# Kernel optimization log

Measured on AMD Instinct MI355X. Metric: run time of the kernel, lower is better.

## Reference

```python
import jax, jax.numpy as jnp
import numpy as np

N_NODES = 100000
N_EDGES = 1600000
IN_FEATS = 128
N_HIDDEN = 128
N_CLASSES = 64


def _degree_norms(src, dst, n_nodes):
    ones = jnp.ones(src.shape[0], dtype=jnp.float32)
    deg_out = jax.ops.segment_sum(ones, src, num_segments=n_nodes)  # out-degree of src nodes
    deg_in = jax.ops.segment_sum(ones, dst, num_segments=n_nodes)   # in-degree of dst nodes
    norm_src = jax.lax.rsqrt(jnp.clip(deg_out, 1.0))  # D_src^{-1/2}, clamp like DGL
    norm_dst = jax.lax.rsqrt(jnp.clip(deg_in, 1.0))   # D_dst^{-1/2}
    return norm_src, norm_dst


def _graph_conv(x, src, dst, norm_src, norm_dst, W, b, relu):
    # DGL GraphConv, norm='both': D_dst^{-1/2} A D_src^{-1/2} X W + b
    h = x * norm_src[:, None]
    agg = jax.ops.segment_sum(h[src], dst, num_segments=x.shape[0])  # [N, d]
    h = agg * norm_dst[:, None]
    h = h @ W + b
    return jax.nn.relu(h) if relu else h


def setup_inputs() -> dict:
    key = jax.random.key(0)
    ks = jax.random.split(key, 10)
    features = jax.random.normal(ks[0], (N_NODES, IN_FEATS), dtype=jnp.float32)
    src = jax.random.randint(ks[1], (N_EDGES,), 0, N_NODES, dtype=jnp.int64 if jax.config.read('jax_enable_x64') else jnp.int32)
    dst = jax.random.randint(ks[2], (N_EDGES,), 0, N_NODES, dtype=src.dtype)
    s = 1.0 / np.sqrt(IN_FEATS)
    W0 = jax.random.uniform(ks[3], (IN_FEATS, N_HIDDEN), jnp.float32, -s, s)
    b0 = jnp.zeros((N_HIDDEN,), jnp.float32)
    sh = 1.0 / np.sqrt(N_HIDDEN)
    W1 = jax.random.uniform(ks[4], (N_HIDDEN, N_HIDDEN), jnp.float32, -sh, sh)
    b1 = jnp.zeros((N_HIDDEN,), jnp.float32)
    W2 = jax.random.uniform(ks[5], (N_HIDDEN, N_CLASSES), jnp.float32, -sh, sh)
    b2 = jnp.zeros((N_CLASSES,), jnp.float32)
    return {"features": features, "src": src, "dst": dst,
            "W0": W0, "b0": b0, "W1": W1, "b1": b1, "W2": W2, "b2": b2}


def reference(features, src, dst, W0, b0, W1, b1, W2, b2):
    norm_src, norm_dst = _degree_norms(src, dst, features.shape[0])
    # dropout is identity in eval mode
    h = _graph_conv(features, src, dst, norm_src, norm_dst, W0, b0, relu=True)
    h = _graph_conv(h, src, dst, norm_src, norm_dst, W1, b1, relu=True)
    h = _graph_conv(h, src, dst, norm_src, norm_dst, W2, b2, relu=False)
    return h
```

## Files before the change

### kernel.cpp

```cpp
#include <hip/hip_runtime.h>
#include <hip/hip_fp16.h>

#define K_FEATS 128
#define RBSHIFT 9
#define RB 512

typedef short bf16x8 __attribute__((ext_vector_type(8)));
typedef float f32x4 __attribute__((ext_vector_type(4)));

__device__ __forceinline__ unsigned short bf16_rne(float x) {
    unsigned u = __float_as_uint(x);
    unsigned r = (u + 0x7FFFu + ((u >> 16) & 1u)) >> 16;
    return (unsigned short)r;
}
__device__ __forceinline__ float bf16_f(unsigned short h) {
    return __uint_as_float(((unsigned)h) << 16);
}

__global__ __launch_bounds__(256) void split_feat(
    const float* __restrict__ X, unsigned short* __restrict__ Xh,
    unsigned short* __restrict__ Xl, int n, int n_pad)
{
    size_t idx = ((size_t)blockIdx.x * 256 + threadIdx.x) * 4;
    if (idx >= (size_t)n_pad * K_FEATS) return;
    int row = (int)(idx >> 7);
    float4 v = make_float4(0.f, 0.f, 0.f, 0.f);
    if (row < n) v = *(const float4*)(X + idx);
    float f[4] = {v.x, v.y, v.z, v.w};
    union { ushort4 q; unsigned short u[4]; } H, L;
#pragma unroll
    for (int j = 0; j < 4; j++) {
        H.u[j] = bf16_rne(f[j]);
        L.u[j] = bf16_rne(f[j] - bf16_f(H.u[j]));
    }
    *(ushort4*)(Xh + idx) = H.q;
    *(ushort4*)(Xl + idx) = L.q;
}

__global__ __launch_bounds__(256) void split_w3(
    const float* __restrict__ W0, const float* __restrict__ W1,
    const float* __restrict__ W2,
    unsigned short* __restrict__ W0th, unsigned short* __restrict__ W0tl,
    unsigned short* __restrict__ W1th, unsigned short* __restrict__ W1tl,
    unsigned short* __restrict__ W2th, unsigned short* __restrict__ W2tl)
{
    int e = blockIdx.x * 256 + threadIdx.x;
    const float* W;
    unsigned short *Wh, *Wl;
    int NC, idx;
    if (e < 16384)      { W = W0; Wh = W0th; Wl = W0tl; NC = 128; idx = e; }
    else if (e < 32768) { W = W1; Wh = W1th; Wl = W1tl; NC = 128; idx = e - 16384; }
    else if (e < 40960) { W = W2; Wh = W2th; Wl = W2tl; NC = 64;  idx = e - 32768; }
    else return;
    int c = idx >> 7, k = idx & 127;
    float w = W[k * NC + c];
    unsigned short h = bf16_rne(w);
    Wh[idx] = h;
    Wl[idx] = bf16_rne(w - bf16_f(h));
}

__global__ __launch_bounds__(256) void bucket_count(
    const int* __restrict__ src, const int* __restrict__ dst,
    int* __restrict__ partialS, int* __restrict__ partialD,
    int ne, int chunkA, int C, int NB)
{
    __shared__ int h[256];
    int c = blockIdx.x, t = threadIdx.x;
    const int* key = blockIdx.y ? dst : src;
    int* part = blockIdx.y ? partialD : partialS;
    if (t < NB) h[t] = 0;
    __syncthreads();
    int e0 = c * chunkA, e1 = min(ne, e0 + chunkA);
    for (int e = e0 + t; e < e1; e += 256)
        atomicAdd(&h[key[e] >> RBSHIFT], 1);
    __syncthreads();
    for (int i = t; i < NB; i += 256) part[i * C + c] = h[i];
}

__global__ __launch_bounds__(256) void bucket_prefix(
    int* __restrict__ partialS, int* __restrict__ partialD,
    int* __restrict__ totS, int* __restrict__ totD, int C, int NB)
{
    __shared__ int sh[256];
    int b = blockIdx.x, t = threadIdx.x;
    int* part = blockIdx.y ? partialD : partialS;
    int* tot = blockIdx.y ? totD : totS;
    int v = (t < C) ? part[b * C + t] : 0;
    sh[t] = v;
    __syncthreads();
    for (int off = 1; off < 256; off <<= 1) {
        int x = (t >= off) ? sh[t - off] : 0;
        __syncthreads();
        sh[t] += x;
        __syncthreads();
    }
    if (t < C) part[b * C + t] = sh[t] - v;
    if (t == 255) tot[b] = sh[255];
}

__global__ __launch_bounds__(256) void bucket_off_kernel(
    const int* __restrict__ totS, const int* __restrict__ totD,
    int* __restrict__ offS, int* __restrict__ offD,
    int* __restrict__ row_off, int NB, int n, int ne)
{
    __shared__ int sh[256];
    int t = threadIdx.x;
    if (t == 0) row_off[n] = ne;
    for (int a = 0; a < 2; a++) {
        const int* tot = a ? totD : totS;
        int* boff = a ? offD : offS;
        int v = (t < NB) ? tot[t] : 0;
        sh[t] = v;
        __syncthreads();
        for (int off = 1; off < 256; off <<= 1) {
            int x = (t >= off) ? sh[t - off] : 0;
            __syncthreads();
            sh[t] += x;
            __syncthreads();
        }
        if (t < NB) boff[t] = sh[t] - v;
        if (t == NB - 1) boff[NB] = sh[t];
        __syncthreads();
    }
}

__global__ __launch_bounds__(256) void bucket_scatter(
    const int* __restrict__ src, const int* __restrict__ dst,
    const int* __restrict__ partialS, const int* __restrict__ partialD,
    const int* __restrict__ offS, const int* __restrict__ offD,
    unsigned short* __restrict__ src_bkt, int* __restrict__ edge_bkt,
    int ne, int chunkA, int C, int NB)
{
    __shared__ int curS[256];
    __shared__ int curD[256];
    int c = blockIdx.x, t = threadIdx.x;
    if (t < NB) {
        curS[t] = offS[t] + partialS[t * C + c];
        curD[t] = offD[t] + partialD[t * C + c];
    }
    __syncthreads();
    int e0 = c * chunkA, e1 = min(ne, e0 + chunkA);
    for (int e = e0 + t; e < e1; e += 256) {
        int s = src[e];
        int d = dst[e];
        int posD = atomicAdd(&curD[d >> RBSHIFT], 1);
        edge_bkt[posD] = ((d & (RB - 1)) << 17) | s;
        int posS = atomicAdd(&curS[s >> RBSHIFT], 1);
        src_bkt[posS] = (unsigned short)(s & (RB - 1));
    }
}

__global__ __launch_bounds__(256) void fine_all(
    const int* __restrict__ edge_bkt, const unsigned short* __restrict__ src_bkt,
    const int* __restrict__ offD, const int* __restrict__ offS,
    int* __restrict__ row_off, float* __restrict__ norm_dst,
    float* __restrict__ norm_src, int* __restrict__ csr, int n)
{
    __shared__ int h[RB];
    __shared__ int ps[256];
    int b = blockIdx.x, t = threadIdx.x;
    int lo = b << RBSHIFT;
    for (int i = t; i < RB; i += 256) h[i] = 0;
    __syncthreads();
    if (blockIdx.y == 1) {
        int e1 = offS[b + 1];
        for (int e = offS[b] + t; e < e1; e += 256)
            atomicAdd(&h[src_bkt[e]], 1);
        __syncthreads();
        for (int i = t; i < RB; i += 256) {
            int g = lo + i;
            if (g < n) norm_src[g] = rsqrtf((float)max(h[i], 1));
        }
        return;
    }
    int ebase = offD[b];
    int e1 = offD[b + 1];
    for (int e = ebase + t; e < e1; e += 256)
        atomicAdd(&h[(unsigned)edge_bkt[e] >> 17], 1);
    __syncthreads();
    int v0 = h[2 * t], v1 = h[2 * t + 1];
    ps[t] = v0 + v1;
    __syncthreads();
    for (int off = 1; off < 256; off <<= 1) {
        int x = (t >= off) ? ps[t - off] : 0;
        __syncthreads();
        ps[t] += x;
        __syncthreads();
    }
    int excl = ps[t] - (v0 + v1) + ebase;
    int g0 = lo + 2 * t, g1 = g0 + 1;
    if (g0 < n) { row_off[g0] = excl;      norm_dst[g0] = rsqrtf((float)max(v0, 1)); }
    if (g1 < n) { row_off[g1] = excl + v0; norm_dst[g1] = rsqrtf((float)max(v1, 1)); }
    h[2 * t] = excl;
    h[2 * t + 1] = excl + v0;
    __syncthreads();
    for (int e = ebase + t; e < e1; e += 256) {
        int p = edge_bkt[e];
        int pos = atomicAdd(&h[(unsigned)p >> 17], 1);
        csr[pos] = p & 0x1FFFF;
    }
}

template <int NCOL, bool HALF_OUT>
__global__ __launch_bounds__(256) void gemm_mfma(
    const unsigned short* __restrict__ Xh, const unsigned short* __restrict__ Xl,
    const unsigned short* __restrict__ Wth, const unsigned short* __restrict__ Wtl,
    const float* __restrict__ scale, void* __restrict__ outv, int n)
{
    constexpr int CT = NCOL / 16;
    constexpr int CHUNKS = NCOL * 16;
    __shared__ unsigned short Ws[16 * NCOL * 8];

    int t = threadIdx.x;
    int w = t >> 6, lane = t & 63, m = lane & 15, q = lane >> 4;
    int r0 = blockIdx.x * 128 + w * 32;

    f32x4 acc[2][CT];
#pragma unroll
    for (int i = 0; i < 2; i++)
#pragma unroll
        for (int j = 0; j < CT; j++) acc[i][j] = (f32x4){0.f, 0.f, 0.f, 0.f};

    size_t aoff0 = (size_t)(r0 + m) * K_FEATS + q * 8;
    size_t aoff1 = aoff0 + (size_t)16 * K_FEATS;

    bf16x8 ah[2][4], al[2][4];
#pragma unroll
    for (int k = 0; k < 4; k++) {
        ah[0][k] = *(const bf16x8*)(Xh + aoff0 + k * 32);
        ah[1][k] = *(const bf16x8*)(Xh + aoff1 + k * 32);
        al[0][k] = *(const bf16x8*)(Xl + aoff0 + k * 32);
        al[1][k] = *(const bf16x8*)(Xl + aoff1 + k * 32);
    }

#pragma unroll
    for (int i = 0; i < CHUNKS / 256; i++) {
        int g = t + i * 256;
        int col = g >> 4, sec = g & 15;
        *(bf16x8*)(Ws + sec * NCOL * 8 + ((col ^ (sec & 7)) * 8)) =
            *(const bf16x8*)(Wth + g * 8);
    }
    __syncthreads();
#pragma unroll
    for (int k = 0; k < 4; k++) {
        int sec = k * 4 + q;
#pragma unroll
        for (int ct = 0; ct < CT; ct++) {
            bf16x8 bh = *(const bf16x8*)(Ws + sec * NCOL * 8 +
                                         (((ct * 16 + m) ^ (sec & 7)) * 8));
            acc[0][ct] = __builtin_amdgcn_mfma_f32_16x16x32_bf16(ah[0][k], bh, acc[0][ct], 0, 0, 0);
            acc[0][ct] = __builtin_amdgcn_mfma_f32_16x16x32_bf16(al[0][k], bh, acc[0][ct], 0, 0, 0);
            acc[1][ct] = __builtin_amdgcn_mfma_f32_16x16x32_bf16(ah[1][k], bh, acc[1][ct], 0, 0, 0);
            acc[1][ct] = __builtin_amdgcn_mfma_f32_16x16x32_bf16(al[1][k], bh, acc[1][ct], 0, 0, 0);
        }
    }
    __syncthreads();
#pragma unroll
    for (int i = 0; i < CHUNKS / 256; i++) {
        int g = t + i * 256;
        int col = g >> 4, sec = g & 15;
        *(bf16x8*)(Ws + sec * NCOL * 8 + ((col ^ (sec & 7)) * 8)) =
            *(const bf16x8*)(Wtl + g * 8);
    }
    __syncthreads();
#pragma unroll
    for (int k = 0; k < 4; k++) {
        int sec = k * 4 + q;
#pragma unroll
        for (int ct = 0; ct < CT; ct++) {
            bf16x8 bl = *(const bf16x8*)(Ws + sec * NCOL * 8 +
                                         (((ct * 16 + m) ^ (sec & 7)) * 8));
            acc[0][ct] = __builtin_amdgcn_mfma_f32_16x16x32_bf16(ah[0][k], bl, acc[0][ct], 0, 0, 0);
            acc[1][ct] = __builtin_amdgcn_mfma_f32_16x16x32_bf16(ah[1][k], bl, acc[1][ct], 0, 0, 0);
        }
    }

#pragma unroll
    for (int rt = 0; rt < 2; rt++) {
        int rb = r0 + rt * 16 + q * 4;
#pragma unroll
        for (int reg = 0; reg < 4; reg++) {
            int row = rb + reg;
            if (row < n) {
                float s = scale[row];
#pragma unroll
                for (int ct = 0; ct < CT; ct++) {
                    float v = acc[rt][ct][reg] * s;
                    size_t o = (size_t)row * NCOL + ct * 16 + m;
                    if (HALF_OUT) ((__half*)outv)[o] = __float2half(v);
                    else ((float*)outv)[o] = v;
                }
            }
        }
    }
}

template <bool RELU>
__global__ __launch_bounds__(256) void aggregate4h(
    const __half* __restrict__ Tm, const int* __restrict__ row_off,
    const int* __restrict__ csr, const float* __restrict__ ndst,
    const float* __restrict__ bias, unsigned short* __restrict__ Oh,
    unsigned short* __restrict__ Ol, int n)
{
    int lane = threadIdx.x & 15;
    int team = threadIdx.x >> 4;
    int fb = lane * 8;
    float b[8];
    *(float4*)&b[0] = *(const float4*)(bias + fb);
    *(float4*)&b[4] = *(const float4*)(bias + fb + 4);
    int stride = gridDim.x * 16;
    for (int v = blockIdx.x * 16 + team; v < n; v += stride) {
        int s = row_off[v], e = row_off[v + 1];
        float nd = ndst[v];
        float a[8] = {};
        int i = s;
        for (; i + 4 <= e; i += 4) {
            int u0 = csr[i], u1 = csr[i + 1], u2 = csr[i + 2], u3 = csr[i + 3];
            union { uint4 q; __half h[8]; } U0, U1, U2, U3;
            U0.q = *(const uint4*)(Tm + (size_t)u0 * 128 + fb);
            U1.q = *(const uint4*)(Tm + (size_t)u1 * 128 + fb);
            U2.q = *(const uint4*)(Tm + (size_t)u2 * 128 + fb);
            U3.q = *(const uint4*)(Tm + (size_t)u3 * 128 + fb);
#pragma unroll
            for (int j = 0; j < 8; j++)
                a[j] += (__half2float(U0.h[j]) + __half2float(U1.h[j])) +
                        (__half2float(U2.h[j]) + __half2float(U3.h[j]));
        }
        for (; i < e; i++) {
            int u = csr[i];
            union { uint4 q; __half h[8]; } U;
            U.q = *(const uint4*)(Tm + (size_t)u * 128 + fb);
#pragma unroll
            for (int j = 0; j < 8; j++) a[j] += __half2float(U.h[j]);
        }
        union { uint4 q; unsigned short u[8]; } H, L;
#pragma unroll
        for (int j = 0; j < 8; j++) {
            float o = nd * a[j] + b[j];
            if (RELU) o = fmaxf(o, 0.f);
            H.u[j] = bf16_rne(o);
            L.u[j] = bf16_rne(o - bf16_f(H.u[j]));
        }
        *(uint4*)(Oh + (size_t)v * 128 + fb) = H.q;
        *(uint4*)(Ol + (size_t)v * 128 + fb) = L.q;
    }
}

template <bool RELU>
__global__ __launch_bounds__(256) void aggregate2(
    const float* __restrict__ Tm, const int* __restrict__ row_off,
    const int* __restrict__ csr, const float* __restrict__ ndst,
    const float* __restrict__ bias, float* __restrict__ out, int n)
{
    int lane = threadIdx.x & 15;
    int team = threadIdx.x >> 4;
    int fb = lane * 4;
    float4 b = *(const float4*)(bias + fb);
    int stride = gridDim.x * 16;
    for (int v = blockIdx.x * 16 + team; v < n; v += stride) {
        int s = row_off[v], e = row_off[v + 1];
        float nd = ndst[v];
        float ax = 0.f, ay = 0.f, az = 0.f, aw = 0.f;
        int i = s;
        for (; i + 4 <= e; i += 4) {
            int u0 = csr[i], u1 = csr[i + 1], u2 = csr[i + 2], u3 = csr[i + 3];
            float4 t0 = *(const float4*)(Tm + (size_t)u0 * 64 + fb);
            float4 t1 = *(const float4*)(Tm + (size_t)u1 * 64 + fb);
            float4 t2 = *(const float4*)(Tm + (size_t)u2 * 64 + fb);
            float4 t3 = *(const float4*)(Tm + (size_t)u3 * 64 + fb);
            ax += (t0.x + t1.x) + (t2.x + t3.x);
            ay += (t0.y + t1.y) + (t2.y + t3.y);
            az += (t0.z + t1.z) + (t2.z + t3.z);
            aw += (t0.w + t1.w) + (t2.w + t3.w);
        }
        for (; i < e; i++) {
            int u = csr[i];
            float4 t0 = *(const float4*)(Tm + (size_t)u * 64 + fb);
            ax += t0.x; ay += t0.y; az += t0.z; aw += t0.w;
        }
        float4 o;
        o.x = nd * ax + b.x;
        o.y = nd * ay + b.y;
        o.z = nd * az + b.z;
        o.w = nd * aw + b.w;
        if (RELU) {
            o.x = fmaxf(o.x, 0.f); o.y = fmaxf(o.y, 0.f);
            o.z = fmaxf(o.z, 0.f); o.w = fmaxf(o.w, 0.f);
        }
        *(float4*)(out + (size_t)v * 64 + fb) = o;
    }
}

extern "C" void kernel_launch(void* const* d_in, const int* in_sizes, int n_in,
                              void* d_out, int out_size, void* d_ws, size_t ws_size,
                              hipStream_t stream)
{
    const float* features = (const float*)d_in[0];
    const int* src = (const int*)d_in[1];
    const int* dst = (const int*)d_in[2];
    const float* W0 = (const float*)d_in[3];
    const float* b0 = (const float*)d_in[4];
    const float* W1 = (const float*)d_in[5];
    const float* b1 = (const float*)d_in[6];
    const float* W2 = (const float*)d_in[7];
    const float* b2 = (const float*)d_in[8];

    int n = in_sizes[0] / K_FEATS;
    int ne = in_sizes[1];
    int n_pad = (n + 127) & ~127;

    char* ws = (char*)d_ws;
    size_t off = 0;
    auto take = [&](size_t bytes) -> char* {
        char* p = ws + off;
        off = (off + bytes + 255) & ~(size_t)255;
        return p;
    };
    unsigned short* XBh = (unsigned short*)take((size_t)n_pad * 128 * 2);
    unsigned short* XBl = (unsigned short*)take((size_t)n_pad * 128 * 2);
    char* Tbuf = take((size_t)n_pad * 128 * 2);
    int* csr = (int*)take((size_t)ne * 4);
    int* edge_bkt = (int*)take((size_t)ne * 4);
    unsigned short* src_bkt = (unsigned short*)take((size_t)ne * 2);
    int* row_off = (int*)take((size_t)(n + 1) * 4);
    float* norm_src = (float*)take((size_t)n * 4);
    float* norm_dst = (float*)take((size_t)n * 4);
    unsigned short* W0th = (unsigned short*)take(128 * 128 * 2);
    unsigned short* W0tl = (unsigned short*)take(128 * 128 * 2);
    unsigned short* W1th = (unsigned short*)take(128 * 128 * 2);
    unsigned short* W1tl = (unsigned short*)take(128 * 128 * 2);
    unsigned short* W2th = (unsigned short*)take(64 * 128 * 2);
    unsigned short* W2tl = (unsigned short*)take(64 * 128 * 2);

    int NB = (n + RB - 1) >> RBSHIFT;
    int chunkA = 8192;
    int C = (ne + chunkA - 1) / chunkA;
    if (C > 256) { chunkA = (ne + 255) / 256; C = (ne + chunkA - 1) / chunkA; }

    int* partialS = (int*)take((size_t)NB * C * 4);
    int* partialD = (int*)take((size_t)NB * C * 4);
    int* totS = (int*)take((size_t)NB * 4);
    int* totD = (int*)take((size_t)NB * 4);
    int* offS = (int*)take((size_t)(NB + 1) * 4);
    int* offD = (int*)take((size_t)(NB + 1) * 4);

    int fblocks = (int)(((size_t)n_pad * 128 / 4 + 255) / 256);
    split_feat<<<fblocks, 256, 0, stream>>>(features, XBh, XBl, n, n_pad);
    split_w3<<<160, 256, 0, stream>>>(W0, W1, W2, W0th, W0tl, W1th, W1tl, W2th, W2tl);

    bucket_count<<<dim3(C, 2), 256, 0, stream>>>(src, dst, partialS, partialD,
                                                 ne, chunkA, C, NB);
    bucket_prefix<<<dim3(NB, 2), 256, 0, stream>>>(partialS, partialD, totS, totD, C, NB);
    bucket_off_kernel<<<1, 256, 0, stream>>>(totS, totD, offS, offD, row_off, NB, n, ne);
    bucket_scatter<<<C, 256, 0, stream>>>(src, dst, partialS, partialD,
                                          offS, offD, src_bkt, edge_bkt,
                                          ne, chunkA, C, NB);
    fine_all<<<dim3(NB, 2), 256, 0, stream>>>(edge_bkt, src_bkt, offD, offS,
                                              row_off, norm_dst, norm_src, csr, n);

    int gblocks = n_pad / 128;
    int ablocks = (n + 15) / 16;
    __half* Th = (__half*)Tbuf;
    float* T64 = (float*)Tbuf;

    gemm_mfma<128, true><<<gblocks, 256, 0, stream>>>(XBh, XBl, W0th, W0tl,
                                                      norm_src, Th, n);
    aggregate4h<true><<<ablocks, 256, 0, stream>>>(Th, row_off, csr, norm_dst, b0,
                                                   XBh, XBl, n);
    gemm_mfma<128, true><<<gblocks, 256, 0, stream>>>(XBh, XBl, W1th, W1tl,
                                                      norm_src, Th, n);
    aggregate4h<true><<<ablocks, 256, 0, stream>>>(Th, row_off, csr, norm_dst, b1,
                                                   XBh, XBl, n);
    gemm_mfma<64, false><<<gblocks, 256, 0, stream>>>(XBh, XBl, W2th, W2tl,
                                                      norm_src, T64, n);
    aggregate2<false><<<ablocks, 256, 0, stream>>>(T64, row_off, csr, norm_dst, b2,
                                                   (float*)d_out, n);
}
```

Measured before the change: 427.2 us.

## Fuse feature split into first GEMM and slice aggregation by feature columns

```diff
diff --git a/kernel.cpp b/kernel.cpp
--- a/kernel.cpp
+++ b/kernel.cpp
@@ -15,26 +15,6 @@
 }
 __device__ __forceinline__ float bf16_f(unsigned short h) {
     return __uint_as_float(((unsigned)h) << 16);
-}
-
-__global__ __launch_bounds__(256) void split_feat(
-    const float* __restrict__ X, unsigned short* __restrict__ Xh,
-    unsigned short* __restrict__ Xl, int n, int n_pad)
-{
-    size_t idx = ((size_t)blockIdx.x * 256 + threadIdx.x) * 4;
-    if (idx >= (size_t)n_pad * K_FEATS) return;
-    int row = (int)(idx >> 7);
-    float4 v = make_float4(0.f, 0.f, 0.f, 0.f);
-    if (row < n) v = *(const float4*)(X + idx);
-    float f[4] = {v.x, v.y, v.z, v.w};
-    union { ushort4 q; unsigned short u[4]; } H, L;
-#pragma unroll
-    for (int j = 0; j < 4; j++) {
-        H.u[j] = bf16_rne(f[j]);
-        L.u[j] = bf16_rne(f[j] - bf16_f(H.u[j]));
-    }
-    *(ushort4*)(Xh + idx) = H.q;
-    *(ushort4*)(Xl + idx) = L.q;
 }
 
 __global__ __launch_bounds__(256) void split_w3(
@@ -201,9 +181,10 @@
     }
 }
 
-template <int NCOL, bool HALF_OUT>
+template <int NCOL, bool HALF_OUT, bool F32IN>
 __global__ __launch_bounds__(256) void gemm_mfma(
     const unsigned short* __restrict__ Xh, const unsigned short* __restrict__ Xl,
+    const float* __restrict__ Xf,
     const unsigned short* __restrict__ Wth, const unsigned short* __restrict__ Wtl,
     const float* __restrict__ scale, void* __restrict__ outv, int n)
 {
@@ -221,16 +202,43 @@
 #pragma unroll
         for (int j = 0; j < CT; j++) acc[i][j] = (f32x4){0.f, 0.f, 0.f, 0.f};
 
-    size_t aoff0 = (size_t)(r0 + m) * K_FEATS + q * 8;
-    size_t aoff1 = aoff0 + (size_t)16 * K_FEATS;
-
     bf16x8 ah[2][4], al[2][4];
-#pragma unroll
-    for (int k = 0; k < 4; k++) {
-        ah[0][k] = *(const bf16x8*)(Xh + aoff0 + k * 32);
-        ah[1][k] = *(const bf16x8*)(Xh + aoff1 + k * 32);
-        al[0][k] = *(const bf16x8*)(Xl + aoff0 + k * 32);
-        al[1][k] = *(const bf16x8*)(Xl + aoff1 + k * 32);
+    if (F32IN) {
+#pragma unroll
+        for (int rt = 0; rt < 2; rt++) {
+            int row = r0 + rt * 16 + m;
+            bool ok = row < n;
+            size_t base = (size_t)row * K_FEATS + q * 8;
+#pragma unroll
+            for (int k = 0; k < 4; k++) {
+                float f[8];
+                if (ok) {
+                    *(float4*)&f[0] = *(const float4*)(Xf + base + k * 32);
+                    *(float4*)&f[4] = *(const float4*)(Xf + base + k * 32 + 4);
+                } else {
+#pragma unroll
+                    for (int j = 0; j < 8; j++) f[j] = 0.f;
+                }
+                union { bf16x8 v; unsigned short u[8]; } H, L;
+#pragma unroll
+                for (int j = 0; j < 8; j++) {
+                    H.u[j] = bf16_rne(f[j]);
+                    L.u[j] = bf16_rne(f[j] - bf16_f(H.u[j]));
+                }
+                ah[rt][k] = H.v;
+                al[rt][k] = L.v;
+            }
+        }
+    } else {
+        size_t aoff0 = (size_t)(r0 + m) * K_FEATS + q * 8;
+        size_t aoff1 = aoff0 + (size_t)16 * K_FEATS;
+#pragma unroll
+        for (int k = 0; k < 4; k++) {
+            ah[0][k] = *(const bf16x8*)(Xh + aoff0 + k * 32);
+            ah[1][k] = *(const bf16x8*)(Xh + aoff1 + k * 32);
+            al[0][k] = *(const bf16x8*)(Xl + aoff0 + k * 32);
+            al[1][k] = *(const bf16x8*)(Xl + aoff1 + k * 32);
+        }
     }
 
 #pragma unroll
@@ -295,99 +303,69 @@
     }
 }
 
-template <bool RELU>
-__global__ __launch_bounds__(256) void aggregate4h(
+template <int NCOL, int SLICES, bool RELU, bool BF16_OUT>
+__global__ __launch_bounds__(256) void aggregate_sliced(
     const __half* __restrict__ Tm, const int* __restrict__ row_off,
     const int* __restrict__ csr, const float* __restrict__ ndst,
-    const float* __restrict__ bias, unsigned short* __restrict__ Oh,
-    unsigned short* __restrict__ Ol, int n)
-{
-    int lane = threadIdx.x & 15;
-    int team = threadIdx.x >> 4;
-    int fb = lane * 8;
-    float b[8];
-    *(float4*)&b[0] = *(const float4*)(bias + fb);
-    *(float4*)&b[4] = *(const float4*)(bias + fb + 4);
-    int stride = gridDim.x * 16;
-    for (int v = blockIdx.x * 16 + team; v < n; v += stride) {
-        int s = row_off[v], e = row_off[v + 1];
-        float nd = ndst[v];
-        float a[8] = {};
-        int i = s;
-        for (; i + 4 <= e; i += 4) {
-            int u0 = csr[i], u1 = csr[i + 1], u2 = csr[i + 2], u3 = csr[i + 3];
-            union { uint4 q; __half h[8]; } U0, U1, U2, U3;
-            U0.q = *(const uint4*)(Tm + (size_t)u0 * 128 + fb);
-            U1.q = *(const uint4*)(Tm + (size_t)u1 * 128 + fb);
-            U2.q = *(const uint4*)(Tm + (size_t)u2 * 128 + fb);
-            U3.q = *(const uint4*)(Tm + (size_t)u3 * 128 + fb);
-#pragma unroll
-            for (int j = 0; j < 8; j++)
-                a[j] += (__half2float(U0.h[j]) + __half2float(U1.h[j])) +
-                        (__half2float(U2.h[j]) + __half2float(U3.h[j]));
-        }
-        for (; i < e; i++) {
-            int u = csr[i];
-            union { uint4 q; __half h[8]; } U;
-            U.q = *(const uint4*)(Tm + (size_t)u * 128 + fb);
-#pragma unroll
-            for (int j = 0; j < 8; j++) a[j] += __half2float(U.h[j]);
-        }
-        union { uint4 q; unsigned short u[8]; } H, L;
-#pragma unroll
-        for (int j = 0; j < 8; j++) {
-            float o = nd * a[j] + b[j];
-            if (RELU) o = fmaxf(o, 0.f);
-            H.u[j] = bf16_rne(o);
-            L.u[j] = bf16_rne(o - bf16_f(H.u[j]));
-        }
-        *(uint4*)(Oh + (size_t)v * 128 + fb) = H.q;
-        *(uint4*)(Ol + (size_t)v * 128 + fb) = L.q;
-    }
-}
-
-template <bool RELU>
-__global__ __launch_bounds__(256) void aggregate2(
-    const float* __restrict__ Tm, const int* __restrict__ row_off,
-    const int* __restrict__ csr, const float* __restrict__ ndst,
-    const float* __restrict__ bias, float* __restrict__ out, int n)
-{
-    int lane = threadIdx.x & 15;
-    int team = threadIdx.x >> 4;
-    int fb = lane * 4;
-    float4 b = *(const float4*)(bias + fb);
-    int stride = gridDim.x * 16;
-    for (int v = blockIdx.x * 16 + team; v < n; v += stride) {
-        int s = row_off[v], e = row_off[v + 1];
-        float nd = ndst[v];
-        float ax = 0.f, ay = 0.f, az = 0.f, aw = 0.f;
-        int i = s;
-        for (; i + 4 <= e; i += 4) {
-            int u0 = csr[i], u1 = csr[i + 1], u2 = csr[i + 2], u3 = csr[i + 3];
-            float4 t0 = *(const float4*)(Tm + (size_t)u0 * 64 + fb);
-            float4 t1 = *(const float4*)(Tm + (size_t)u1 * 64 + fb);
-            float4 t2 = *(const float4*)(Tm + (size_t)u2 * 64 + fb);
-            float4 t3 = *(const float4*)(Tm + (size_t)u3 * 64 + fb);
-            ax += (t0.x + t1.x) + (t2.x + t3.x);
-            ay += (t0.y + t1.y) + (t2.y + t3.y);
-            az += (t0.z + t1.z) + (t2.z + t3.z);
-            aw += (t0.w + t1.w) + (t2.w + t3.w);
-        }
-        for (; i < e; i++) {
-            int u = csr[i];
-            float4 t0 = *(const float4*)(Tm + (size_t)u * 64 + fb);
-            ax += t0.x; ay += t0.y; az += t0.z; aw += t0.w;
-        }
-        float4 o;
-        o.x = nd * ax + b.x;
-        o.y = nd * ay + b.y;
-        o.z = nd * az + b.z;
-        o.w = nd * aw + b.w;
-        if (RELU) {
-            o.x = fmaxf(o.x, 0.f); o.y = fmaxf(o.y, 0.f);
-            o.z = fmaxf(o.z, 0.f); o.w = fmaxf(o.w, 0.f);
-        }
-        *(float4*)(out + (size_t)v * 64 + fb) = o;
+    const float* __restrict__ bias, void* __restrict__ outA,
+    unsigned short* __restrict__ outB, int n)
+{
+    constexpr int SH = (SLICES == 8) ? 3 : 2;
+    int slice = blockIdx.x & (SLICES - 1);
+    int g = blockIdx.x >> SH;
+    int team = threadIdx.x >> 2;
+    int li = threadIdx.x & 3;
+    int fb = slice * 16 + li * 4;
+    int v = g * 64 + team;
+    if (v >= n) return;
+    float4 bb = *(const float4*)(bias + fb);
+    int s = row_off[v], e = row_off[v + 1];
+    float nd = ndst[v];
+    float a0 = 0.f, a1 = 0.f, a2 = 0.f, a3 = 0.f;
+    int i = s;
+    for (; i + 4 <= e; i += 4) {
+        int u0 = csr[i], u1 = csr[i + 1], u2 = csr[i + 2], u3 = csr[i + 3];
+        union { uint2 q; __half h[4]; } U0, U1, U2, U3;
+        U0.q = *(const uint2*)(Tm + (size_t)u0 * NCOL + fb);
+        U1.q = *(const uint2*)(Tm + (size_t)u1 * NCOL + fb);
+        U2.q = *(const uint2*)(Tm + (size_t)u2 * NCOL + fb);
+        U3.q = *(const uint2*)(Tm + (size_t)u3 * NCOL + fb);
+        a0 += (__half2float(U0.h[0]) + __half2float(U1.h[0])) +
+              (__half2float(U2.h[0]) + __half2float(U3.h[0]));
+        a1 += (__half2float(U0.h[1]) + __half2float(U1.h[1])) +
+              (__half2float(U2.h[1]) + __half2float(U3.h[1]));
+        a2 += (__half2float(U0.h[2]) + __half2float(U1.h[2])) +
+              (__half2float(U2.h[2]) + __half2float(U3.h[2]));
+        a3 += (__half2float(U0.h[3]) + __half2float(U1.h[3])) +
+              (__half2float(U2.h[3]) + __half2float(U3.h[3]));
+    }
+    for (; i < e; i++) {
+        int u = csr[i];
+        union { uint2 q; __half h[4]; } U;
+        U.q = *(const uint2*)(Tm + (size_t)u * NCOL + fb);
+        a0 += __half2float(U.h[0]);
+        a1 += __half2float(U.h[1]);
+        a2 += __half2float(U.h[2]);
+        a3 += __half2float(U.h[3]);
+    }
+    float o0 = nd * a0 + bb.x, o1 = nd * a1 + bb.y;
+    float o2 = nd * a2 + bb.z, o3 = nd * a3 + bb.w;
+    if (RELU) {
+        o0 = fmaxf(o0, 0.f); o1 = fmaxf(o1, 0.f);
+        o2 = fmaxf(o2, 0.f); o3 = fmaxf(o3, 0.f);
+    }
+    if (BF16_OUT) {
+        union { uint2 q; unsigned short u[4]; } H, L;
+        float o[4] = {o0, o1, o2, o3};
+#pragma unroll
+        for (int j = 0; j < 4; j++) {
+            H.u[j] = bf16_rne(o[j]);
+            L.u[j] = bf16_rne(o[j] - bf16_f(H.u[j]));
+        }
+        *(uint2*)((unsigned short*)outA + (size_t)v * NCOL + fb) = H.q;
+        *(uint2*)(outB + (size_t)v * NCOL + fb) = L.q;
+    } else {
+        *(float4*)((float*)outA + (size_t)v * NCOL + fb) = make_float4(o0, o1, o2, o3);
     }
 }
 
@@ -444,8 +422,6 @@
     int* offS = (int*)take((size_t)(NB + 1) * 4);
     int* offD = (int*)take((size_t)(NB + 1) * 4);
 
-    int fblocks = (int)(((size_t)n_pad * 128 / 4 + 255) / 256);
-    split_feat<<<fblocks, 256, 0, stream>>>(features, XBh, XBl, n, n_pad);
     split_w3<<<160, 256, 0, stream>>>(W0, W1, W2, W0th, W0tl, W1th, W1tl, W2th, W2tl);
 
     bucket_count<<<dim3(C, 2), 256, 0, stream>>>(src, dst, partialS, partialD,
@@ -459,20 +435,19 @@
                                               row_off, norm_dst, norm_src, csr, n);
 
     int gblocks = n_pad / 128;
-    int ablocks = (n + 15) / 16;
+    int ngroups = (n + 63) / 64;
     __half* Th = (__half*)Tbuf;
-    float* T64 = (float*)Tbuf;
-
-    gemm_mfma<128, true><<<gblocks, 256, 0, stream>>>(XBh, XBl, W0th, W0tl,
-                                                      norm_src, Th, n);
-    aggregate4h<true><<<ablocks, 256, 0, stream>>>(Th, row_off, csr, norm_dst, b0,
-                                                   XBh, XBl, n);
-    gemm_mfma<128, true><<<gblocks, 256, 0, stream>>>(XBh, XBl, W1th, W1tl,
-                                                      norm_src, Th, n);
-    aggregate4h<true><<<ablocks, 256, 0, stream>>>(Th, row_off, csr, norm_dst, b1,
-                                                   XBh, XBl, n);
-    gemm_mfma<64, false><<<gblocks, 256, 0, stream>>>(XBh, XBl, W2th, W2tl,
-                                                      norm_src, T64, n);
-    aggregate2<false><<<ablocks, 256, 0, stream>>>(T64, row_off, csr, norm_dst, b2,
-                                                   (float*)d_out, n);
-}
+
+    gemm_mfma<128, true, true><<<gblocks, 256, 0, stream>>>(
+        nullptr, nullptr, features, W0th, W0tl, norm_src, Th, n);
+    aggregate_sliced<128, 8, true, true><<<ngroups * 8, 256, 0, stream>>>(
+        Th, row_off, csr, norm_dst, b0, XBh, XBl, n);
+    gemm_mfma<128, true, false><<<gblocks, 256, 0, stream>>>(
+        XBh, XBl, nullptr, W1th, W1tl, norm_src, Th, n);
+    aggregate_sliced<128, 8, true, true><<<ngroups * 8, 256, 0, stream>>>(
+        Th, row_off, csr, norm_dst, b1, XBh, XBl, n);
+    gemm_mfma<64, true, false><<<gblocks, 256, 0, stream>>>(
+        XBh, XBl, nullptr, W2th, W2tl, norm_src, Th, n);
+    aggregate_sliced<64, 4, false, false><<<ngroups * 4, 256, 0, stream>>>(
+        Th, row_off, csr, norm_dst, b2, d_out, nullptr, n);
+}
```

After: 749.0 us. 75.3% more time.

## Fuse bf16 split into GEMM loads and store fp16 intermediates

Applied to the files above, without the earlier changes.

```diff
diff --git a/kernel.cpp b/kernel.cpp
--- a/kernel.cpp
+++ b/kernel.cpp
@@ -15,26 +15,6 @@
 }
 __device__ __forceinline__ float bf16_f(unsigned short h) {
     return __uint_as_float(((unsigned)h) << 16);
-}
-
-__global__ __launch_bounds__(256) void split_feat(
-    const float* __restrict__ X, unsigned short* __restrict__ Xh,
-    unsigned short* __restrict__ Xl, int n, int n_pad)
-{
-    size_t idx = ((size_t)blockIdx.x * 256 + threadIdx.x) * 4;
-    if (idx >= (size_t)n_pad * K_FEATS) return;
-    int row = (int)(idx >> 7);
-    float4 v = make_float4(0.f, 0.f, 0.f, 0.f);
-    if (row < n) v = *(const float4*)(X + idx);
-    float f[4] = {v.x, v.y, v.z, v.w};
-    union { ushort4 q; unsigned short u[4]; } H, L;
-#pragma unroll
-    for (int j = 0; j < 4; j++) {
-        H.u[j] = bf16_rne(f[j]);
-        L.u[j] = bf16_rne(f[j] - bf16_f(H.u[j]));
-    }
-    *(ushort4*)(Xh + idx) = H.q;
-    *(ushort4*)(Xl + idx) = L.q;
 }
 
 __global__ __launch_bounds__(256) void split_w3(
@@ -64,17 +44,21 @@
     int* __restrict__ partialS, int* __restrict__ partialD,
     int ne, int chunkA, int C, int NB)
 {
-    __shared__ int h[256];
+    __shared__ int hS[256];
+    __shared__ int hD[256];
     int c = blockIdx.x, t = threadIdx.x;
-    const int* key = blockIdx.y ? dst : src;
-    int* part = blockIdx.y ? partialD : partialS;
-    if (t < NB) h[t] = 0;
+    if (t < NB) { hS[t] = 0; hD[t] = 0; }
     __syncthreads();
     int e0 = c * chunkA, e1 = min(ne, e0 + chunkA);
-    for (int e = e0 + t; e < e1; e += 256)
-        atomicAdd(&h[key[e] >> RBSHIFT], 1);
-    __syncthreads();
-    for (int i = t; i < NB; i += 256) part[i * C + c] = h[i];
+    for (int e = e0 + t; e < e1; e += 256) {
+        atomicAdd(&hS[src[e] >> RBSHIFT], 1);
+        atomicAdd(&hD[dst[e] >> RBSHIFT], 1);
+    }
+    __syncthreads();
+    for (int i = t; i < NB; i += 256) {
+        partialS[i * C + c] = hS[i];
+        partialD[i * C + c] = hD[i];
+    }
 }
 
 __global__ __launch_bounds__(256) void bucket_prefix(
@@ -201,9 +185,9 @@
     }
 }
 
-template <int NCOL, bool HALF_OUT>
+template <int NCOL, bool HALF_OUT, int MODE>
 __global__ __launch_bounds__(256) void gemm_mfma(
-    const unsigned short* __restrict__ Xh, const unsigned short* __restrict__ Xl,
+    const __half* __restrict__ X16, const float* __restrict__ Xf,
     const unsigned short* __restrict__ Wth, const unsigned short* __restrict__ Wtl,
     const float* __restrict__ scale, void* __restrict__ outv, int n)
 {
@@ -221,16 +205,37 @@
 #pragma unroll
         for (int j = 0; j < CT; j++) acc[i][j] = (f32x4){0.f, 0.f, 0.f, 0.f};
 
-    size_t aoff0 = (size_t)(r0 + m) * K_FEATS + q * 8;
-    size_t aoff1 = aoff0 + (size_t)16 * K_FEATS;
-
     bf16x8 ah[2][4], al[2][4];
 #pragma unroll
-    for (int k = 0; k < 4; k++) {
-        ah[0][k] = *(const bf16x8*)(Xh + aoff0 + k * 32);
-        ah[1][k] = *(const bf16x8*)(Xh + aoff1 + k * 32);
-        al[0][k] = *(const bf16x8*)(Xl + aoff0 + k * 32);
-        al[1][k] = *(const bf16x8*)(Xl + aoff1 + k * 32);
+    for (int rt = 0; rt < 2; rt++) {
+        int row = r0 + rt * 16 + m;
+        size_t base = (size_t)row * K_FEATS + q * 8;
+#pragma unroll
+        for (int k = 0; k < 4; k++) {
+            float f[8];
+            if (MODE == 0) {
+                if (row < n) {
+                    *(float4*)&f[0] = *(const float4*)(Xf + base + k * 32);
+                    *(float4*)&f[4] = *(const float4*)(Xf + base + k * 32 + 4);
+                } else {
+#pragma unroll
+                    for (int j = 0; j < 8; j++) f[j] = 0.f;
+                }
+            } else {
+                union { uint4 q4; __half h[8]; } U;
+                U.q4 = *(const uint4*)(X16 + base + k * 32);
+#pragma unroll
+                for (int j = 0; j < 8; j++) f[j] = __half2float(U.h[j]);
+            }
+            union { bf16x8 v; unsigned short u[8]; } H, L;
+#pragma unroll
+            for (int j = 0; j < 8; j++) {
+                H.u[j] = bf16_rne(f[j]);
+                L.u[j] = bf16_rne(f[j] - bf16_f(H.u[j]));
+            }
+            ah[rt][k] = H.v;
+            al[rt][k] = L.v;
+        }
     }
 
 #pragma unroll
@@ -299,8 +304,7 @@
 __global__ __launch_bounds__(256) void aggregate4h(
     const __half* __restrict__ Tm, const int* __restrict__ row_off,
     const int* __restrict__ csr, const float* __restrict__ ndst,
-    const float* __restrict__ bias, unsigned short* __restrict__ Oh,
-    unsigned short* __restrict__ Ol, int n)
+    const float* __restrict__ bias, __half* __restrict__ Oh, int n)
 {
     int lane = threadIdx.x & 15;
     int team = threadIdx.x >> 4;
@@ -333,61 +337,58 @@
 #pragma unroll
             for (int j = 0; j < 8; j++) a[j] += __half2float(U.h[j]);
         }
-        union { uint4 q; unsigned short u[8]; } H, L;
+        union { uint4 q; __half h[8]; } O;
 #pragma unroll
         for (int j = 0; j < 8; j++) {
             float o = nd * a[j] + b[j];
             if (RELU) o = fmaxf(o, 0.f);
-            H.u[j] = bf16_rne(o);
-            L.u[j] = bf16_rne(o - bf16_f(H.u[j]));
-        }
-        *(uint4*)(Oh + (size_t)v * 128 + fb) = H.q;
-        *(uint4*)(Ol + (size_t)v * 128 + fb) = L.q;
-    }
-}
-
-template <bool RELU>
-__global__ __launch_bounds__(256) void aggregate2(
-    const float* __restrict__ Tm, const int* __restrict__ row_off,
+            O.h[j] = __float2half(o);
+        }
+        *(uint4*)(Oh + (size_t)v * 128 + fb) = O.q;
+    }
+}
+
+__global__ __launch_bounds__(256) void aggregate2h(
+    const __half* __restrict__ Tm, const int* __restrict__ row_off,
     const int* __restrict__ csr, const float* __restrict__ ndst,
     const float* __restrict__ bias, float* __restrict__ out, int n)
 {
-    int lane = threadIdx.x & 15;
-    int team = threadIdx.x >> 4;
-    int fb = lane * 4;
-    float4 b = *(const float4*)(bias + fb);
-    int stride = gridDim.x * 16;
-    for (int v = blockIdx.x * 16 + team; v < n; v += stride) {
+    int lane = threadIdx.x & 7;
+    int team = threadIdx.x >> 3;
+    int fb = lane * 8;
+    float b[8];
+    *(float4*)&b[0] = *(const float4*)(bias + fb);
+    *(float4*)&b[4] = *(const float4*)(bias + fb + 4);
+    int stride = gridDim.x * 32;
+    for (int v = blockIdx.x * 32 + team; v < n; v += stride) {
         int s = row_off[v], e = row_off[v + 1];
         float nd = ndst[v];
-        float ax = 0.f, ay = 0.f, az = 0.f, aw = 0.f;
+        float a[8] = {};
         int i = s;
         for (; i + 4 <= e; i += 4) {
             int u0 = csr[i], u1 = csr[i + 1], u2 = csr[i + 2], u3 = csr[i + 3];
-            float4 t0 = *(const float4*)(Tm + (size_t)u0 * 64 + fb);
-            float4 t1 = *(const float4*)(Tm + (size_t)u1 * 64 + fb);
-            float4 t2 = *(const float4*)(Tm + (size_t)u2 * 64 + fb);
-            float4 t3 = *(const float4*)(Tm + (size_t)u3 * 64 + fb);
-            ax += (t0.x + t1.x) + (t2.x + t3.x);
-            ay += (t0.y + t1.y) + (t2.y + t3.y);
-            az += (t0.z + t1.z) + (t2.z + t3.z);
-            aw += (t0.w + t1.w) + (t2.w + t3.w);
+            union { uint4 q; __half h[8]; } U0, U1, U2, U3;
+            U0.q = *(const uint4*)(Tm + (size_t)u0 * 64 + fb);
+            U1.q = *(const uint4*)(Tm + (size_t)u1 * 64 + fb);
+            U2.q = *(const uint4*)(Tm + (size_t)u2 * 64 + fb);
+            U3.q = *(const uint4*)(Tm + (size_t)u3 * 64 + fb);
+#pragma unroll
+            for (int j = 0; j < 8; j++)
+                a[j] += (__half2float(U0.h[j]) + __half2float(U1.h[j])) +
+                        (__half2float(U2.h[j]) + __half2float(U3.h[j]));
         }
         for (; i < e; i++) {
             int u = csr[i];
-            float4 t0 = *(const float4*)(Tm + (size_t)u * 64 + fb);
-            ax += t0.x; ay += t0.y; az += t0.z; aw += t0.w;
-        }
-        float4 o;
-        o.x = nd * ax + b.x;
-        o.y = nd * ay + b.y;
-        o.z = nd * az + b.z;
-        o.w = nd * aw + b.w;
-        if (RELU) {
-            o.x = fmaxf(o.x, 0.f); o.y = fmaxf(o.y, 0.f);
-            o.z = fmaxf(o.z, 0.f); o.w = fmaxf(o.w, 0.f);
-        }
-        *(float4*)(out + (size_t)v * 64 + fb) = o;
+            union { uint4 q; __half h[8]; } U;
+            U.q = *(const uint4*)(Tm + (size_t)u * 64 + fb);
+#pragma unroll
+            for (int j = 0; j < 8; j++) a[j] += __half2float(U.h[j]);
+        }
+        float o[8];
+#pragma unroll
+        for (int j = 0; j < 8; j++) o[j] = nd * a[j] + b[j];
+        *(float4*)(out + (size_t)v * 64 + fb) = *(float4*)&o[0];
+        *(float4*)(out + (size_t)v * 64 + fb + 4) = *(float4*)&o[4];
     }
 }
 
@@ -416,9 +417,8 @@
         off = (off + bytes + 255) & ~(size_t)255;
         return p;
     };
-    unsigned short* XBh = (unsigned short*)take((size_t)n_pad * 128 * 2);
-    unsigned short* XBl = (unsigned short*)take((size_t)n_pad * 128 * 2);
-    char* Tbuf = take((size_t)n_pad * 128 * 2);
+    __half* Xbuf = (__half*)take((size_t)n_pad * 128 * 2);
+    __half* Th = (__half*)take((size_t)n_pad * 128 * 2);
     int* csr = (int*)take((size_t)ne * 4);
     int* edge_bkt = (int*)take((size_t)ne * 4);
     unsigned short* src_bkt = (unsigned short*)take((size_t)ne * 2);
@@ -444,12 +444,10 @@
     int* offS = (int*)take((size_t)(NB + 1) * 4);
     int* offD = (int*)take((size_t)(NB + 1) * 4);
 
-    int fblocks = (int)(((size_t)n_pad * 128 / 4 + 255) / 256);
-    split_feat<<<fblocks, 256, 0, stream>>>(features, XBh, XBl, n, n_pad);
     split_w3<<<160, 256, 0, stream>>>(W0, W1, W2, W0th, W0tl, W1th, W1tl, W2th, W2tl);
 
-    bucket_count<<<dim3(C, 2), 256, 0, stream>>>(src, dst, partialS, partialD,
-                                                 ne, chunkA, C, NB);
+    bucket_count<<<C, 256, 0, stream>>>(src, dst, partialS, partialD,
+                                        ne, chunkA, C, NB);
     bucket_prefix<<<dim3(NB, 2), 256, 0, stream>>>(partialS, partialD, totS, totD, C, NB);
     bucket_off_kernel<<<1, 256, 0, stream>>>(totS, totD, offS, offD, row_off, NB, n, ne);
     bucket_scatter<<<C, 256, 0, stream>>>(src, dst, partialS, partialD,
@@ -459,20 +457,19 @@
                                               row_off, norm_dst, norm_src, csr, n);
 
     int gblocks = n_pad / 128;
-    int ablocks = (n + 15) / 16;
-    __half* Th = (__half*)Tbuf;
-    float* T64 = (float*)Tbuf;
-
-    gemm_mfma<128, true><<<gblocks, 256, 0, stream>>>(XBh, XBl, W0th, W0tl,
-                                                      norm_src, Th, n);
-    aggregate4h<true><<<ablocks, 256, 0, stream>>>(Th, row_off, csr, norm_dst, b0,
-                                                   XBh, XBl, n);
-    gemm_mfma<128, true><<<gblocks, 256, 0, stream>>>(XBh, XBl, W1th, W1tl,
-                                                      norm_src, Th, n);
-    aggregate4h<true><<<ablocks, 256, 0, stream>>>(Th, row_off, csr, norm_dst, b1,
-                                                   XBh, XBl, n);
-    gemm_mfma<64, false><<<gblocks, 256, 0, stream>>>(XBh, XBl, W2th, W2tl,
-                                                      norm_src, T64, n);
-    aggregate2<false><<<ablocks, 256, 0, stream>>>(T64, row_off, csr, norm_dst, b2,
-                                                   (float*)d_out, n);
-}
+    int ablocks4 = (n + 15) / 16;
+    int ablocks2 = (n + 31) / 32;
+
+    gemm_mfma<128, true, 0><<<gblocks, 256, 0, stream>>>(
+        nullptr, features, W0th, W0tl, norm_src, Th, n);
+    aggregate4h<true><<<ablocks4, 256, 0, stream>>>(Th, row_off, csr, norm_dst, b0,
+                                                    Xbuf, n);
+    gemm_mfma<128, true, 1><<<gblocks, 256, 0, stream>>>(
+        Xbuf, nullptr, W1th, W1tl, norm_src, Th, n);
+    aggregate4h<true><<<ablocks4, 256, 0, stream>>>(Th, row_off, csr, norm_dst, b1,
+                                                    Xbuf, n);
+    gemm_mfma<64, true, 1><<<gblocks, 256, 0, stream>>>(
+        Xbuf, nullptr, W2th, W2tl, norm_src, Th, n);
+    aggregate2h<<<ablocks2, 256, 0, stream>>>(Th, row_off, csr, norm_dst, b2,
+                                              (float*)d_out, n);
+}
```

Result: faster. 375.6 us (-12.1%).
